# Performance work log

Measured on AMD Instinct MI355X. Metric: run time of the kernel, lower is better.

## Reference

```python
import jax, jax.numpy as jnp
import numpy as np

N_NODES = 100000
N_EDGES = 1600000
MAX_RADIUS = 3.0
NUM_BASIS = 3
SQRT2 = 2.0 ** 0.5
# e3nn soft_one_hot_linspace 'smooth_finite' prefactor
C_SMOOTH = 1.14136 * float(np.exp(2.0))


def _sus(x):
    # smooth unit step: exp(-1/x) for x>0 else 0 (NaN-safe for grad)
    safe = jnp.where(x > 0.0, x, 1.0)
    return jnp.where(x > 0.0, jnp.exp(-1.0 / safe), 0.0)


def radial_embed(d):
    # soft_one_hot_linspace(d, 0, max_radius, 3, basis='smooth_finite', cutoff=True) * sqrt(num_basis)
    values = jnp.linspace(0.0, MAX_RADIUS, NUM_BASIS + 2)[1:-1]  # [3]
    step = MAX_RADIUS / (NUM_BASIS + 1)
    diff = (d[:, None] - values) / step  # [E,3]
    y = C_SMOOTH * _sus(diff + 1.0) * _sus(1.0 - diff)
    return y * (NUM_BASIS ** 0.5)


def fcnet(x, w1, w2):
    # e3nn FullyConnectedNet([3,16,numel], relu): normalized weights, normalize2mom(relu)=sqrt(2)*relu
    h = SQRT2 * jax.nn.relu(x @ (w1 / w1.shape[0] ** 0.5))
    return h @ (w2 / w2.shape[0] ** 0.5)


def reference(pos, feat, edge_src, edge_dst, fc1_w1, fc1_w2, core_w1, core_w2, fc3_w1, fc3_w2, conv_w, conv_b):
    n = pos.shape[0]
    z = edge_src.shape[0] / n  # average num neighbors
    edge_vec = pos[edge_dst] - pos[edge_src]
    d = jnp.sqrt(jnp.sum(edge_vec * edge_vec, axis=1))  # edges are self-loop-free -> d > 0
    emb = radial_embed(d)  # [E,3]

    # NOTE on e3nn math: with input/mid/output parities all even and sh = 0e+1o+2e,
    # the only parity-allowed paths producing nonzero output are the 0e (scalar) paths,
    # which contract against Y_0 = 1 ('component' normalization). The 4x1e block of the
    # mid irreps is identically zero (no parity-allowed path ever populates it), so the
    # math below (scalar block only, with e3nn path weights) is exactly equivalent.
    def conv(x, w1, w2, mul_in, mul_out, path_w):
        # per-edge weights from radial MLP; keep the 0e->0e instruction block
        w = fcnet(emb, w1, w2)[:, : mul_in * mul_out].reshape(-1, mul_in, mul_out)
        msg = path_w * jnp.einsum('euw,eu->ew', w, x[edge_src])
        return jax.ops.segment_sum(msg, edge_dst, num_segments=n) / z ** 0.5

    x = conv(feat, fc1_w1, fc1_w2, 3, 4, (1.0 / 3.0) ** 0.5)  # tp1: fan_in 3*1 -> pw=1/sqrt(3)
    for i in range(3):
        x = conv(x, core_w1[i], core_w2[i], 4, 4, 0.5)  # tp2 0e path: pw=sqrt(1/4)
    x = conv(x, fc3_w1, fc3_w2, 4, 16, 0.5)  # tp3: pw=sqrt(1/4)
    # Conv1d(16, 2, 1) == pointwise linear
    return x @ conv_w.T + conv_b


def setup_inputs():
    key = jax.random.key(0)
    ks = jax.random.split(key, 12)
    pos = jax.random.uniform(ks[0], (N_NODES, 3), dtype=jnp.float32)  # unit box -> all edge lengths < max_radius
    feat = jax.random.normal(ks[1], (N_NODES, 3), dtype=jnp.float32)
    edge_src = jax.random.randint(ks[2], (N_EDGES,), 0, N_NODES, dtype=jnp.int32)
    off = jax.random.randint(ks[3], (N_EDGES,), 1, N_NODES, dtype=jnp.int32)
    edge_dst = ((edge_src + off) % N_NODES).astype(jnp.int32)  # radius_graph has no self-loops
    return {
        'pos': pos,
        'feat': feat,
        'edge_src': edge_src,
        'edge_dst': edge_dst,
        'fc1_w1': jax.random.normal(ks[4], (3, 16), jnp.float32),
        'fc1_w2': jax.random.normal(ks[5], (16, 12), jnp.float32),
        'core_w1': jax.random.normal(ks[6], (3, 3, 16), jnp.float32),
        'core_w2': jax.random.normal(ks[7], (3, 16, 48), jnp.float32),
        'fc3_w1': jax.random.normal(ks[8], (3, 16), jnp.float32),
        'fc3_w2': jax.random.normal(ks[9], (16, 64), jnp.float32),
        'conv_w': jax.random.normal(ks[10], (2, 16), jnp.float32) * 0.25,
        'conv_b': jax.random.normal(ks[11], (2,), jnp.float32) * 0.1,
    }
```

## Files before the change

kernel.cpp:

```cpp
#include <hip/hip_runtime.h>


#define BCAP 4608
#define NBMAX 400

__device__ __forceinline__ float sus_f(float x) {
    return x > 0.0f ? __expf(-1.0f / x) : 0.0f;
}

__device__ __forceinline__ float uload(const float* p) {
    return __uint_as_float(__builtin_amdgcn_readfirstlane(__float_as_uint(*p)));
}

__global__ __launch_bounds__(256) void k_bin(
    const int* __restrict__ src, const int* __restrict__ dst,
    int* __restrict__ gcur, int* __restrict__ ptmp,
    const float* __restrict__ fc3w2, const float* __restrict__ cw,
    float* __restrict__ gbuf,
    int nedges, int nb)
{
    __shared__ int cnt[NBMAX];
    __shared__ int gb[NBMAX];
    for (int b = threadIdx.x; b < nb; b += 256) cnt[b] = 0;
    __syncthreads();

    int base = blockIdx.x * 2048 + threadIdx.x * 8;
    int pk[8]; int bk[8]; short r[8];
    int ss[8], dd[8];
    if (base + 7 < nedges) {
        int4 s0 = *(const int4*)&src[base];
        int4 s1 = *(const int4*)&src[base + 4];
        int4 d0 = *(const int4*)&dst[base];
        int4 d1 = *(const int4*)&dst[base + 4];
        ss[0]=s0.x; ss[1]=s0.y; ss[2]=s0.z; ss[3]=s0.w;
        ss[4]=s1.x; ss[5]=s1.y; ss[6]=s1.z; ss[7]=s1.w;
        dd[0]=d0.x; dd[1]=d0.y; dd[2]=d0.z; dd[3]=d0.w;
        dd[4]=d1.x; dd[5]=d1.y; dd[6]=d1.z; dd[7]=d1.w;
        #pragma unroll
        for (int i = 0; i < 8; ++i) {
            int b = dd[i] >> 8;
            bk[i] = b;
            pk[i] = (ss[i] << 8) | (dd[i] & 255);
            r[i] = (short)atomicAdd(&cnt[b], 1);
        }
    } else {
        #pragma unroll
        for (int i = 0; i < 8; ++i) {
            int e = base + i;
            if (e < nedges) {
                int s = src[e], t = dst[e];
                int b = t >> 8;
                bk[i] = b;
                pk[i] = (s << 8) | (t & 255);
                r[i] = (short)atomicAdd(&cnt[b], 1);
            } else bk[i] = -1;
        }
    }
    __syncthreads();
    for (int b = threadIdx.x; b < nb; b += 256) {
        int c = cnt[b];
        gb[b] = c > 0 ? atomicAdd(&gcur[b], c) : 0;
    }
    __syncthreads();
    #pragma unroll
    for (int i = 0; i < 8; ++i) {
        if (bk[i] >= 0) {
            int p = gb[bk[i]] + (int)r[i];
            if (p < BCAP)
                ptmp[bk[i] * BCAP + p] = pk[i];
        }
    }

    if (blockIdx.x == 0 && threadIdx.x < 128) {
        int idx = threadIdx.x;
        int k = idx >> 3, u = (idx >> 1) & 3, c = idx & 1;
        float s = 0.0f;
        #pragma unroll
        for (int w = 0; w < 16; ++w)
            s = fmaf(fc3w2[k * 64 + u * 16 + w], cw[c * 16 + w], s);
        gbuf[idx] = s;
    }
}

__global__ __launch_bounds__(1024) void k_build(
    const int* __restrict__ gcur, const int* __restrict__ ptmp,
    const float* __restrict__ pos,
    float4* __restrict__ ebuf, int2* __restrict__ offs2,
    int n, int nb)
{
    int b = blockIdx.x;
    int cnt = gcur[b]; if (cnt > BCAP) cnt = BCAP;
    int t = threadIdx.x;

    __shared__ int stage[BCAP];
    __shared__ int perm[BCAP];
    __shared__ int deg[256];
    __shared__ int loffs[256];
    __shared__ int cur[256];

    const int* tin = ptmp + b * BCAP;
    for (int j = t; j < cnt; j += 1024) stage[j] = tin[j];
    if (t < 256) deg[t] = 0;
    __syncthreads();

    for (int j = t; j < cnt; j += 1024)
        atomicAdd(&deg[stage[j] & 255], 1);
    __syncthreads();

    if (t < 64) {
        int d0 = deg[4 * t + 0], d1 = deg[4 * t + 1];
        int d2 = deg[4 * t + 2], d3 = deg[4 * t + 3];
        int s = d0 + d1 + d2 + d3;
        int x = s;
        #pragma unroll
        for (int off = 1; off < 64; off <<= 1) {
            int y = __shfl_up(x, off);
            if (t >= off) x += y;
        }
        int ex = x - s;
        int e0 = ex, e1 = ex + d0, e2 = e1 + d1, e3 = e2 + d2;
        loffs[4 * t + 0] = e0; cur[4 * t + 0] = e0;
        loffs[4 * t + 1] = e1; cur[4 * t + 1] = e1;
        loffs[4 * t + 2] = e2; cur[4 * t + 2] = e2;
        loffs[4 * t + 3] = e3; cur[4 * t + 3] = e3;
    }
    __syncthreads();

    int nid0 = b << 8;
    {
        int nn = n - nid0; if (nn > 256) nn = 256;
        if (t < nn) {
            int st = b * BCAP + loffs[t];
            offs2[nid0 + t] = make_int2(st, st + deg[t]);
        }
    }

    for (int j = t; j < cnt; j += 1024) {
        int pkd = stage[j];
        perm[atomicAdd(&cur[pkd & 255], 1)] = pkd;
    }
    __syncthreads();

    const float C = 1.14136f * 7.3890560989306495f;
    for (int j = t; j < cnt; j += 1024) {
        int pkd = perm[j];
        int s = pkd >> 8;
        int tt = nid0 | (pkd & 255);
        float dx = pos[3 * tt + 0] - pos[3 * s + 0];
        float dy = pos[3 * tt + 1] - pos[3 * s + 1];
        float dz = pos[3 * tt + 2] - pos[3 * s + 2];
        float d = sqrtf(dx * dx + dy * dy + dz * dz);
        float e0, e1, e2;
        { float f = (d - 0.75f) * (1.0f / 0.75f);
          e0 = C * sus_f(f + 1.0f) * sus_f(1.0f - f); }
        { float f = (d - 1.50f) * (1.0f / 0.75f);
          e1 = C * sus_f(f + 1.0f) * sus_f(1.0f - f); }
        { float f = (d - 2.25f) * (1.0f / 0.75f);
          e2 = C * sus_f(f + 1.0f) * sus_f(1.0f - f); }
        ebuf[(size_t)b * BCAP + j] = make_float4(__int_as_float(s), e0, e1, e2);
    }
}


__global__ __launch_bounds__(256) void k_node_l1(
    const float* __restrict__ feat, const float4* __restrict__ edata,
    const int2* __restrict__ offs2,
    const float* __restrict__ w1, const float* __restrict__ w2,
    float* __restrict__ xout, int n)
{
    __shared__ float lw[16 * 20];
    if (threadIdx.x < 192) {
        int k = threadIdx.x / 12, r = threadIdx.x % 12;
        lw[k * 20 + r] = w2[k * 12 + r];
    }
    __syncthreads();

    int g = blockIdx.x * 256 + threadIdx.x;
    int nd = g >> 2;
    if (nd >= n) return;
    int t = g & 3;

    float w1r[3][16];
    #pragma unroll
    for (int j = 0; j < 3; ++j)
        #pragma unroll
        for (int k = 0; k < 16; ++k) w1r[j][k] = uload(&w1[j * 16 + k]);

    float O[16][3];
    #pragma unroll
    for (int k = 0; k < 16; ++k)
        #pragma unroll
        for (int u = 0; u < 3; ++u) O[k][u] = 0.0f;

    int2 se = offs2[nd];
    for (int e = se.x + t; e < se.y; e += 4) {
        float4 ed = edata[e];
        int s = __float_as_int(ed.x);
        float f0 = feat[3 * s + 0], f1 = feat[3 * s + 1], f2 = feat[3 * s + 2];
        #pragma unroll
        for (int k = 0; k < 16; ++k) {
            float a = fmaf(ed.y, w1r[0][k], fmaf(ed.z, w1r[1][k], ed.w * w1r[2][k]));
            float h = a > 0.0f ? a : 0.0f;
            O[k][0] = fmaf(h, f0, O[k][0]);
            O[k][1] = fmaf(h, f1, O[k][1]);
            O[k][2] = fmaf(h, f2, O[k][2]);
        }
    }

    float p0 = 0.f, p1 = 0.f, p2 = 0.f, p3 = 0.f;
    #pragma unroll
    for (int k = 0; k < 16; ++k)
        #pragma unroll
        for (int u = 0; u < 3; ++u) {
            const float4 q = *(const float4*)&lw[k * 20 + u * 4];
            float o = O[k][u];
            p0 = fmaf(o, q.x, p0); p1 = fmaf(o, q.y, p1);
            p2 = fmaf(o, q.z, p2); p3 = fmaf(o, q.w, p3);
        }
    p0 += __shfl_xor(p0, 1); p1 += __shfl_xor(p1, 1);
    p2 += __shfl_xor(p2, 1); p3 += __shfl_xor(p3, 1);
    p0 += __shfl_xor(p0, 2); p1 += __shfl_xor(p1, 2);
    p2 += __shfl_xor(p2, 2); p3 += __shfl_xor(p3, 2);
    if (t == 0) {
        const float S = 0.051031036307982884f;
        float4 o; o.x = p0 * S; o.y = p1 * S; o.z = p2 * S; o.w = p3 * S;
        ((float4*)xout)[nd] = o;
    }
}

__global__ __launch_bounds__(256) void k_node_core(
    const float4* __restrict__ xin, const float4* __restrict__ edata,
    const int2* __restrict__ offs2,
    const float* __restrict__ w1, const float* __restrict__ w2,
    float* __restrict__ xout, int n)
{
    __shared__ float lw[16 * 20];
    {
        int idx = threadIdx.x;
        int k = idx >> 4, r = idx & 15;
        lw[k * 20 + r] = w2[k * 48 + r];
    }
    __syncthreads();

    int g = blockIdx.x * 256 + threadIdx.x;
    int nd = g >> 2;
    if (nd >= n) return;
    int t = g & 3;

    float w1r[3][16];
    #pragma unroll
    for (int j = 0; j < 3; ++j)
        #pragma unroll
        for (int k = 0; k < 16; ++k) w1r[j][k] = uload(&w1[j * 16 + k]);

    float O[16][4];
    #pragma unroll
    for (int k = 0; k < 16; ++k)
        #pragma unroll
        for (int u = 0; u < 4; ++u) O[k][u] = 0.0f;

    int2 se = offs2[nd];
    for (int e = se.x + t; e < se.y; e += 4) {
        float4 ed = edata[e];
        int s = __float_as_int(ed.x);
        float4 x = xin[s];
        #pragma unroll
        for (int k = 0; k < 16; ++k) {
            float a = fmaf(ed.y, w1r[0][k], fmaf(ed.z, w1r[1][k], ed.w * w1r[2][k]));
            float h = a > 0.0f ? a : 0.0f;
            O[k][0] = fmaf(h, x.x, O[k][0]);
            O[k][1] = fmaf(h, x.y, O[k][1]);
            O[k][2] = fmaf(h, x.z, O[k][2]);
            O[k][3] = fmaf(h, x.w, O[k][3]);
        }
    }

    float p0 = 0.f, p1 = 0.f, p2 = 0.f, p3 = 0.f;
    #pragma unroll
    for (int k = 0; k < 16; ++k)
        #pragma unroll
        for (int u = 0; u < 4; ++u) {
            const float4 q = *(const float4*)&lw[k * 20 + u * 4];
            float o = O[k][u];
            p0 = fmaf(o, q.x, p0); p1 = fmaf(o, q.y, p1);
            p2 = fmaf(o, q.z, p2); p3 = fmaf(o, q.w, p3);
        }
    p0 += __shfl_xor(p0, 1); p1 += __shfl_xor(p1, 1);
    p2 += __shfl_xor(p2, 1); p3 += __shfl_xor(p3, 1);
    p0 += __shfl_xor(p0, 2); p1 += __shfl_xor(p1, 2);
    p2 += __shfl_xor(p2, 2); p3 += __shfl_xor(p3, 2);
    if (t == 0) {
        const float S = 0.04419417382415922f;
        float4 o; o.x = p0 * S; o.y = p1 * S; o.z = p2 * S; o.w = p3 * S;
        ((float4*)xout)[nd] = o;
    }
}

__global__ __launch_bounds__(256) void k_node_fc3_final(
    const float4* __restrict__ xin, const float4* __restrict__ edata,
    const int2* __restrict__ offs2,
    const float* __restrict__ w1, const float* __restrict__ gbuf,
    const float* __restrict__ cb,
    float* __restrict__ out, int n)
{
    __shared__ float lg[128];
    if (threadIdx.x < 128) lg[threadIdx.x] = gbuf[threadIdx.x];
    __syncthreads();

    int g = blockIdx.x * 256 + threadIdx.x;
    int nd = g >> 2;
    if (nd >= n) return;
    int t = g & 3;

    float w1r[3][16];
    #pragma unroll
    for (int j = 0; j < 3; ++j)
        #pragma unroll
        for (int k = 0; k < 16; ++k) w1r[j][k] = uload(&w1[j * 16 + k]);

    float O[16][4];
    #pragma unroll
    for (int k = 0; k < 16; ++k)
        #pragma unroll
        for (int u = 0; u < 4; ++u) O[k][u] = 0.0f;

    int2 se = offs2[nd];
    for (int e = se.x + t; e < se.y; e += 4) {
        float4 ed = edata[e];
        int s = __float_as_int(ed.x);
        float4 x = xin[s];
        #pragma unroll
        for (int k = 0; k < 16; ++k) {
            float a = fmaf(ed.y, w1r[0][k], fmaf(ed.z, w1r[1][k], ed.w * w1r[2][k]));
            float h = a > 0.0f ? a : 0.0f;
            O[k][0] = fmaf(h, x.x, O[k][0]);
            O[k][1] = fmaf(h, x.y, O[k][1]);
            O[k][2] = fmaf(h, x.z, O[k][2]);
            O[k][3] = fmaf(h, x.w, O[k][3]);
        }
    }

    float a0 = 0.f, a1 = 0.f;
    #pragma unroll
    for (int k = 0; k < 16; ++k)
        #pragma unroll
        for (int u = 0; u < 4; ++u) {
            float o = O[k][u];
            const float2 q = *(const float2*)&lg[(k * 4 + u) * 2];
            a0 = fmaf(o, q.x, a0);
            a1 = fmaf(o, q.y, a1);
        }
    a0 += __shfl_xor(a0, 1); a1 += __shfl_xor(a1, 1);
    a0 += __shfl_xor(a0, 2); a1 += __shfl_xor(a1, 2);
    if (t == 0) {
        const float S = 0.04419417382415922f;
        float2 o; o.x = fmaf(a0, S, cb[0]); o.y = fmaf(a1, S, cb[1]);
        ((float2*)out)[nd] = o;
    }
}


extern "C" void kernel_launch(void* const* d_in, const int* in_sizes, int n_in,
                              void* d_out, int out_size, void* d_ws, size_t ws_size,
                              hipStream_t stream) {
    const float* pos     = (const float*)d_in[0];
    const float* feat    = (const float*)d_in[1];
    const int*   esrc    = (const int*)d_in[2];
    const int*   edst    = (const int*)d_in[3];
    const float* fc1_w1  = (const float*)d_in[4];
    const float* fc1_w2  = (const float*)d_in[5];
    const float* core_w1 = (const float*)d_in[6];
    const float* core_w2 = (const float*)d_in[7];
    const float* fc3_w1  = (const float*)d_in[8];
    const float* fc3_w2  = (const float*)d_in[9];
    const float* conv_w  = (const float*)d_in[10];
    const float* conv_b  = (const float*)d_in[11];
    float* out = (float*)d_out;

    const int E = in_sizes[2];
    const int N = in_sizes[0] / 3;
    const int nb = (N + 255) >> 8;

    float4* ebuf = (float4*)d_ws;
    int* ptmp  = (int*)(ebuf + (size_t)nb * BCAP);
    float* xa  = (float*)(ptmp + (size_t)nb * BCAP);
    float* xb  = xa + (size_t)4 * N;
    int2* offs2 = (int2*)(xb + (size_t)4 * N);
    int* gcur  = (int*)(offs2 + N);
    float* gbuf = (float*)(gcur + ((nb + 3) & ~3));

    int g4 = (4 * N + 255) / 256;

    hipMemsetAsync(gcur, 0, (size_t)nb * sizeof(int), stream);
    k_bin<<<(E + 2047) / 2048, 256, 0, stream>>>(esrc, edst, gcur, ptmp,
                                                 fc3_w2, conv_w, gbuf, E, nb);
    k_build<<<nb, 1024, 0, stream>>>(gcur, ptmp, pos, ebuf, offs2, N, nb);

    k_node_l1<<<g4, 256, 0, stream>>>(feat, ebuf, offs2, fc1_w1, fc1_w2, xa, N);
    k_node_core<<<g4, 256, 0, stream>>>((const float4*)xa, ebuf, offs2,
                                        core_w1 + 0, core_w2 + 0, xb, N);
    k_node_core<<<g4, 256, 0, stream>>>((const float4*)xb, ebuf, offs2,
                                        core_w1 + 48, core_w2 + 768, xa, N);
    k_node_core<<<g4, 256, 0, stream>>>((const float4*)xa, ebuf, offs2,
                                        core_w1 + 96, core_w2 + 1536, xb, N);
    k_node_fc3_final<<<g4, 256, 0, stream>>>((const float4*)xb, ebuf, offs2,
                                             fc3_w1, gbuf, conv_b, out, N);
}
```

Measured before the change: 233.0 us.

## Replace two-pass bucket sort with direct per-node slot scatter via atomics

Drops the bin kernel and the per-bucket counting-sort build kernel. A single scatter kernel now takes a slot for each edge with a global atomic on a per-node counter and writes the edge's source index and radial embedding into a fixed 64-entry slot array for its destination node. The node kernels read a per-node degree instead of offset pairs. This removes a kernel launch and an intermediate buffer pass, at the cost of random global atomics, uncoalesced 16-byte writes, a much larger edge buffer, and silently dropping edges for any node with more than 64 incoming edges.

```diff
diff --git a/kernel.cpp b/kernel.cpp
--- a/kernel.cpp
+++ b/kernel.cpp
@@ -1,8 +1,7 @@
 #include <hip/hip_runtime.h>
 
 
-#define BCAP 4608
-#define NBMAX 400
+#define DCAP 64
 
 __device__ __forceinline__ float sus_f(float x) {
     return x > 0.0f ? __expf(-1.0f / x) : 0.0f;
@@ -12,20 +11,16 @@
     return __uint_as_float(__builtin_amdgcn_readfirstlane(__float_as_uint(*p)));
 }
 
-__global__ __launch_bounds__(256) void k_bin(
+__global__ __launch_bounds__(256) void k_scatter(
     const int* __restrict__ src, const int* __restrict__ dst,
-    int* __restrict__ gcur, int* __restrict__ ptmp,
+    const float* __restrict__ pos,
+    int* __restrict__ dcur, float4* __restrict__ ebuf,
     const float* __restrict__ fc3w2, const float* __restrict__ cw,
     float* __restrict__ gbuf,
-    int nedges, int nb)
+    int nedges)
 {
-    __shared__ int cnt[NBMAX];
-    __shared__ int gb[NBMAX];
-    for (int b = threadIdx.x; b < nb; b += 256) cnt[b] = 0;
-    __syncthreads();
-
+    const float C = 1.14136f * 7.3890560989306495f;
     int base = blockIdx.x * 2048 + threadIdx.x * 8;
-    int pk[8]; int bk[8]; short r[8];
     int ss[8], dd[8];
     if (base + 7 < nedges) {
         int4 s0 = *(const int4*)&src[base];
@@ -36,119 +31,23 @@
         ss[4]=s1.x; ss[5]=s1.y; ss[6]=s1.z; ss[7]=s1.w;
         dd[0]=d0.x; dd[1]=d0.y; dd[2]=d0.z; dd[3]=d0.w;
         dd[4]=d1.x; dd[5]=d1.y; dd[6]=d1.z; dd[7]=d1.w;
-        #pragma unroll
-        for (int i = 0; i < 8; ++i) {
-            int b = dd[i] >> 8;
-            bk[i] = b;
-            pk[i] = (ss[i] << 8) | (dd[i] & 255);
-            r[i] = (short)atomicAdd(&cnt[b], 1);
-        }
     } else {
         #pragma unroll
         for (int i = 0; i < 8; ++i) {
             int e = base + i;
-            if (e < nedges) {
-                int s = src[e], t = dst[e];
-                int b = t >> 8;
-                bk[i] = b;
-                pk[i] = (s << 8) | (t & 255);
-                r[i] = (short)atomicAdd(&cnt[b], 1);
-            } else bk[i] = -1;
-        }
-    }
-    __syncthreads();
-    for (int b = threadIdx.x; b < nb; b += 256) {
-        int c = cnt[b];
-        gb[b] = c > 0 ? atomicAdd(&gcur[b], c) : 0;
-    }
-    __syncthreads();
+            if (e < nedges) { ss[i] = src[e]; dd[i] = dst[e]; }
+            else dd[i] = -1;
+        }
+    }
+
     #pragma unroll
     for (int i = 0; i < 8; ++i) {
-        if (bk[i] >= 0) {
-            int p = gb[bk[i]] + (int)r[i];
-            if (p < BCAP)
-                ptmp[bk[i] * BCAP + p] = pk[i];
-        }
-    }
-
-    if (blockIdx.x == 0 && threadIdx.x < 128) {
-        int idx = threadIdx.x;
-        int k = idx >> 3, u = (idx >> 1) & 3, c = idx & 1;
-        float s = 0.0f;
-        #pragma unroll
-        for (int w = 0; w < 16; ++w)
-            s = fmaf(fc3w2[k * 64 + u * 16 + w], cw[c * 16 + w], s);
-        gbuf[idx] = s;
-    }
-}
-
-__global__ __launch_bounds__(1024) void k_build(
-    const int* __restrict__ gcur, const int* __restrict__ ptmp,
-    const float* __restrict__ pos,
-    float4* __restrict__ ebuf, int2* __restrict__ offs2,
-    int n, int nb)
-{
-    int b = blockIdx.x;
-    int cnt = gcur[b]; if (cnt > BCAP) cnt = BCAP;
-    int t = threadIdx.x;
-
-    __shared__ int stage[BCAP];
-    __shared__ int perm[BCAP];
-    __shared__ int deg[256];
-    __shared__ int loffs[256];
-    __shared__ int cur[256];
-
-    const int* tin = ptmp + b * BCAP;
-    for (int j = t; j < cnt; j += 1024) stage[j] = tin[j];
-    if (t < 256) deg[t] = 0;
-    __syncthreads();
-
-    for (int j = t; j < cnt; j += 1024)
-        atomicAdd(&deg[stage[j] & 255], 1);
-    __syncthreads();
-
-    if (t < 64) {
-        int d0 = deg[4 * t + 0], d1 = deg[4 * t + 1];
-        int d2 = deg[4 * t + 2], d3 = deg[4 * t + 3];
-        int s = d0 + d1 + d2 + d3;
-        int x = s;
-        #pragma unroll
-        for (int off = 1; off < 64; off <<= 1) {
-            int y = __shfl_up(x, off);
-            if (t >= off) x += y;
-        }
-        int ex = x - s;
-        int e0 = ex, e1 = ex + d0, e2 = e1 + d1, e3 = e2 + d2;
-        loffs[4 * t + 0] = e0; cur[4 * t + 0] = e0;
-        loffs[4 * t + 1] = e1; cur[4 * t + 1] = e1;
-        loffs[4 * t + 2] = e2; cur[4 * t + 2] = e2;
-        loffs[4 * t + 3] = e3; cur[4 * t + 3] = e3;
-    }
-    __syncthreads();
-
-    int nid0 = b << 8;
-    {
-        int nn = n - nid0; if (nn > 256) nn = 256;
-        if (t < nn) {
-            int st = b * BCAP + loffs[t];
-            offs2[nid0 + t] = make_int2(st, st + deg[t]);
-        }
-    }
-
-    for (int j = t; j < cnt; j += 1024) {
-        int pkd = stage[j];
-        perm[atomicAdd(&cur[pkd & 255], 1)] = pkd;
-    }
-    __syncthreads();
-
-    const float C = 1.14136f * 7.3890560989306495f;
-    for (int j = t; j < cnt; j += 1024) {
-        int pkd = perm[j];
-        int s = pkd >> 8;
-        int tt = nid0 | (pkd & 255);
-        float dx = pos[3 * tt + 0] - pos[3 * s + 0];
-        float dy = pos[3 * tt + 1] - pos[3 * s + 1];
-        float dz = pos[3 * tt + 2] - pos[3 * s + 2];
+        if (dd[i] < 0) continue;
+        int t = dd[i], s = ss[i];
+        int r = atomicAdd(&dcur[t], 1);
+        float dx = pos[3 * t + 0] - pos[3 * s + 0];
+        float dy = pos[3 * t + 1] - pos[3 * s + 1];
+        float dz = pos[3 * t + 2] - pos[3 * s + 2];
         float d = sqrtf(dx * dx + dy * dy + dz * dz);
         float e0, e1, e2;
         { float f = (d - 0.75f) * (1.0f / 0.75f);
@@ -157,14 +56,25 @@
           e1 = C * sus_f(f + 1.0f) * sus_f(1.0f - f); }
         { float f = (d - 2.25f) * (1.0f / 0.75f);
           e2 = C * sus_f(f + 1.0f) * sus_f(1.0f - f); }
-        ebuf[(size_t)b * BCAP + j] = make_float4(__int_as_float(s), e0, e1, e2);
+        if (r < DCAP)
+            ebuf[((size_t)t << 6) + r] = make_float4(__int_as_float(s), e0, e1, e2);
+    }
+
+    if (blockIdx.x == 0 && threadIdx.x < 128) {
+        int idx = threadIdx.x;
+        int k = idx >> 3, u = (idx >> 1) & 3, c = idx & 1;
+        float s = 0.0f;
+        #pragma unroll
+        for (int w = 0; w < 16; ++w)
+            s = fmaf(fc3w2[k * 64 + u * 16 + w], cw[c * 16 + w], s);
+        gbuf[idx] = s;
     }
 }
 
 
 __global__ __launch_bounds__(256) void k_node_l1(
     const float* __restrict__ feat, const float4* __restrict__ edata,
-    const int2* __restrict__ offs2,
+    const int* __restrict__ dcur,
     const float* __restrict__ w1, const float* __restrict__ w2,
     float* __restrict__ xout, int n)
 {
@@ -192,8 +102,9 @@
         #pragma unroll
         for (int u = 0; u < 3; ++u) O[k][u] = 0.0f;
 
-    int2 se = offs2[nd];
-    for (int e = se.x + t; e < se.y; e += 4) {
+    int deg = dcur[nd]; if (deg > DCAP) deg = DCAP;
+    int bse = nd << 6;
+    for (int e = bse + t; e < bse + deg; e += 4) {
         float4 ed = edata[e];
         int s = __float_as_int(ed.x);
         float f0 = feat[3 * s + 0], f1 = feat[3 * s + 1], f2 = feat[3 * s + 2];
@@ -230,7 +141,7 @@
 
 __global__ __launch_bounds__(256) void k_node_core(
     const float4* __restrict__ xin, const float4* __restrict__ edata,
-    const int2* __restrict__ offs2,
+    const int* __restrict__ dcur,
     const float* __restrict__ w1, const float* __restrict__ w2,
     float* __restrict__ xout, int n)
 {
@@ -259,8 +170,9 @@
         #pragma unroll
         for (int u = 0; u < 4; ++u) O[k][u] = 0.0f;
 
-    int2 se = offs2[nd];
-    for (int e = se.x + t; e < se.y; e += 4) {
+    int deg = dcur[nd]; if (deg > DCAP) deg = DCAP;
+    int bse = nd << 6;
+    for (int e = bse + t; e < bse + deg; e += 4) {
         float4 ed = edata[e];
         int s = __float_as_int(ed.x);
         float4 x = xin[s];
@@ -298,7 +210,7 @@
 
 __global__ __launch_bounds__(256) void k_node_fc3_final(
     const float4* __restrict__ xin, const float4* __restrict__ edata,
-    const int2* __restrict__ offs2,
+    const int* __restrict__ dcur,
     const float* __restrict__ w1, const float* __restrict__ gbuf,
     const float* __restrict__ cb,
     float* __restrict__ out, int n)
@@ -324,8 +236,9 @@
         #pragma unroll
         for (int u = 0; u < 4; ++u) O[k][u] = 0.0f;
 
-    int2 se = offs2[nd];
-    for (int e = se.x + t; e < se.y; e += 4) {
+    int deg = dcur[nd]; if (deg > DCAP) deg = DCAP;
+    int bse = nd << 6;
+    for (int e = bse + t; e < bse + deg; e += 4) {
         float4 ed = edata[e];
         int s = __float_as_int(ed.x);
         float4 x = xin[s];
@@ -379,30 +292,26 @@
 
     const int E = in_sizes[2];
     const int N = in_sizes[0] / 3;
-    const int nb = (N + 255) >> 8;
 
     float4* ebuf = (float4*)d_ws;
-    int* ptmp  = (int*)(ebuf + (size_t)nb * BCAP);
-    float* xa  = (float*)(ptmp + (size_t)nb * BCAP);
+    float* xa  = (float*)(ebuf + ((size_t)N << 6));
     float* xb  = xa + (size_t)4 * N;
-    int2* offs2 = (int2*)(xb + (size_t)4 * N);
-    int* gcur  = (int*)(offs2 + N);
-    float* gbuf = (float*)(gcur + ((nb + 3) & ~3));
+    int* dcur  = (int*)(xb + (size_t)4 * N);
+    float* gbuf = (float*)(dcur + ((N + 3) & ~3));
 
     int g4 = (4 * N + 255) / 256;
 
-    hipMemsetAsync(gcur, 0, (size_t)nb * sizeof(int), stream);
-    k_bin<<<(E + 2047) / 2048, 256, 0, stream>>>(esrc, edst, gcur, ptmp,
-                                                 fc3_w2, conv_w, gbuf, E, nb);
-    k_build<<<nb, 1024, 0, stream>>>(gcur, ptmp, pos, ebuf, offs2, N, nb);
-
-    k_node_l1<<<g4, 256, 0, stream>>>(feat, ebuf, offs2, fc1_w1, fc1_w2, xa, N);
-    k_node_core<<<g4, 256, 0, stream>>>((const float4*)xa, ebuf, offs2,
+    hipMemsetAsync(dcur, 0, (size_t)N * sizeof(int), stream);
+    k_scatter<<<(E + 2047) / 2048, 256, 0, stream>>>(esrc, edst, pos, dcur, ebuf,
+                                                     fc3_w2, conv_w, gbuf, E);
+
+    k_node_l1<<<g4, 256, 0, stream>>>(feat, ebuf, dcur, fc1_w1, fc1_w2, xa, N);
+    k_node_core<<<g4, 256, 0, stream>>>((const float4*)xa, ebuf, dcur,
                                         core_w1 + 0, core_w2 + 0, xb, N);
-    k_node_core<<<g4, 256, 0, stream>>>((const float4*)xb, ebuf, offs2,
+    k_node_core<<<g4, 256, 0, stream>>>((const float4*)xb, ebuf, dcur,
                                         core_w1 + 48, core_w2 + 768, xa, N);
-    k_node_core<<<g4, 256, 0, stream>>>((const float4*)xa, ebuf, offs2,
+    k_node_core<<<g4, 256, 0, stream>>>((const float4*)xa, ebuf, dcur,
                                         core_w1 + 96, core_w2 + 1536, xb, N);
-    k_node_fc3_final<<<g4, 256, 0, stream>>>((const float4*)xb, ebuf, offs2,
+    k_node_fc3_final<<<g4, 256, 0, stream>>>((const float4*)xb, ebuf, dcur,
                                              fc3_w1, gbuf, conv_b, out, N);
 }
```

Result: slower. 274.2 us (+17.6%).
